# Kernel tuning notes

Hardware: AMD Instinct MI355X
Metric: run time of the kernel (lower is better)

Reference implementation:

```python
import jax, jax.numpy as jnp
import numpy as np

N = 8192
IN_F = 256
HEADS = 4
HF = 64            # head_features = out_features / heads
OUT_F = HEADS * HF # concat=True
NEG_SLOPE = 0.2


def setup_inputs() -> dict:
    key = jax.random.key(0)
    ks = jax.random.split(key, 7)
    x = jax.random.normal(ks[0], (N, IN_F), dtype=jnp.float32)
    graph = jax.random.randint(ks[1], (N, N), 0, 2, dtype=jnp.int32)
    weight = jax.random.normal(ks[2], (HEADS, IN_F, HF), dtype=jnp.float32) * (1.0 / np.sqrt(IN_F))
    weight_i = jax.random.normal(ks[3], (HEADS, HF, 1), dtype=jnp.float32) * (1.0 / np.sqrt(HF))
    weight_j = jax.random.normal(ks[4], (HEADS, HF, 1), dtype=jnp.float32) * (1.0 / np.sqrt(HF))
    weight_r = jax.random.normal(ks[5], (IN_F, HF * HEADS), dtype=jnp.float32) * (1.0 / np.sqrt(IN_F))
    bias = jnp.zeros((OUT_F,), dtype=jnp.float32)
    return {"x": x, "graph": graph, "weight": weight, "weight_i": weight_i,
            "weight_j": weight_j, "weight_r": weight_r, "bias": bias}


def reference(x, graph, weight, weight_i, weight_j, weight_r, bias):
    # h: per-head projected features [heads, N, hf]
    h = jnp.einsum('nm,hmf->hnf', x, weight)
    # additive attention logits: coe_i [h,N,1] + coe_j [h,1,N]
    coe_i = jnp.einsum('hnf,hfo->hno', h, weight_i)          # [heads, N, 1]
    coe_j = jnp.einsum('hnf,hfo->hno', h, weight_j)          # [heads, N, 1]
    coe = jax.nn.leaky_relu(coe_i + jnp.swapaxes(coe_j, 1, 2), NEG_SLOPE)  # [heads, N, N]
    # adjacency mask (note transpose, matching the torch code)
    mask = jnp.where(graph > 0, 0.0, -jnp.inf).T             # [N, N]
    att = jax.nn.softmax(coe + mask[None], axis=-1)          # [heads, N, N]
    # aggregate and move heads to axis 1: [N, heads, hf]
    y = jnp.einsum('hij,hjf->ihf', att, h)
    # residual with projection (in_features != head_features)
    y = y + (x @ weight_r).reshape(N, HEADS, HF)
    # concat heads + bias
    y = y.reshape(N, OUT_F) + bias
    return y
```

## Files before the change

kernel.cpp:

```cpp
#include <hip/hip_runtime.h>
#include <hip/hip_bf16.h>

#define N 8192
#define IN_F 256
#define HEADS 4
#define HF 64
#define OUT_F 256

typedef __attribute__((ext_vector_type(8))) short short8;
typedef __attribute__((ext_vector_type(4))) float f32x4;

__device__ __forceinline__ float lrelu(float x) {
    return fmaxf(x, 0.0f) * 0.8f + x * 0.2f;
}
__device__ __forceinline__ short f2bf(float f) {
    union { __hip_bfloat16 h; short s; } u;
    u.h = __float2bfloat16(f);
    return u.s;
}
__device__ __forceinline__ float bf2f(unsigned short b) {
    union { unsigned u; float f; } v; v.u = ((unsigned)b) << 16;
    return v.f;
}
__device__ __forceinline__ unsigned pack_bf16(float p0, float p1) {
    union { __hip_bfloat162 b; unsigned u; } cv;
    cv.b = __float22bfloat162_rn(make_float2(p0, p1));
    return cv.u;
}

__global__ __launch_bounds__(256) void k_wcvt(
    const float* __restrict__ w, const float* __restrict__ wr,
    unsigned short* __restrict__ BbT)
{
    int c = blockIdx.x;
    int k = threadIdx.x;
    float v;
    if (c < 256) {
        int head = c >> 6, f = c & 63;
        v = w[((size_t)head * IN_F + k) * HF + f];
    } else {
        v = wr[(size_t)k * OUT_F + (c - 256)];
    }
    BbT[(size_t)c * IN_F + k] = (unsigned short)f2bf(v);
}

__global__ __launch_bounds__(256) void k_gemm(
    const float* __restrict__ x, const unsigned short* __restrict__ BbT,
    const float* __restrict__ bias,
    unsigned short* __restrict__ hT, float* __restrict__ out)
{
    __shared__ unsigned short Asw[64 * 64];
    __shared__ unsigned short Bsw[128 * 64];
    int t = threadIdx.x;
    int m0 = blockIdx.x * 64;
    int bn = blockIdx.y;
    int w_ = t >> 6, l = t & 63;
    int wr_ = w_ >> 1, wc_ = w_ & 1;
    int ar = l & 15, g = l >> 4;

    f32x4 acc[2][4];
    #pragma unroll
    for (int m = 0; m < 2; ++m)
        #pragma unroll
        for (int n = 0; n < 4; ++n) acc[m][n] = (f32x4){0.f, 0.f, 0.f, 0.f};

    int srow = t >> 2, skq = (t & 3) * 16;
    int sc = t >> 1, sh = (t & 1) * 32;

    for (int kt = 0; kt < 4; ++kt) {
        const float* xs = x + (size_t)(m0 + srow) * IN_F + kt * 64 + skq;
        float4 xa = ((const float4*)xs)[0];
        float4 xb = ((const float4*)xs)[1];
        float4 xc = ((const float4*)xs)[2];
        float4 xd = ((const float4*)xs)[3];
        unsigned ae[8];
        ae[0] = pack_bf16(xa.x, xa.y); ae[1] = pack_bf16(xa.z, xa.w);
        ae[2] = pack_bf16(xb.x, xb.y); ae[3] = pack_bf16(xb.z, xb.w);
        ae[4] = pack_bf16(xc.x, xc.y); ae[5] = pack_bf16(xc.z, xc.w);
        ae[6] = pack_bf16(xd.x, xd.y); ae[7] = pack_bf16(xd.z, xd.w);
        int kb0 = (skq >> 3) ^ (srow & 7);
        int kb1 = ((skq >> 3) + 1) ^ (srow & 7);
        *(uint4*)&Asw[srow * 64 + kb0 * 8] = *(uint4*)&ae[0];
        *(uint4*)&Asw[srow * 64 + kb1 * 8] = *(uint4*)&ae[4];
        const unsigned short* bs = BbT + (size_t)(bn * 128 + sc) * IN_F + kt * 64 + sh;
        uint4 b0 = ((const uint4*)bs)[0];
        uint4 b1 = ((const uint4*)bs)[1];
        uint4 b2 = ((const uint4*)bs)[2];
        uint4 b3 = ((const uint4*)bs)[3];
        int hb = sh >> 3;
        *(uint4*)&Bsw[sc * 64 + ((hb + 0) ^ (sc & 7)) * 8] = b0;
        *(uint4*)&Bsw[sc * 64 + ((hb + 1) ^ (sc & 7)) * 8] = b1;
        *(uint4*)&Bsw[sc * 64 + ((hb + 2) ^ (sc & 7)) * 8] = b2;
        *(uint4*)&Bsw[sc * 64 + ((hb + 3) ^ (sc & 7)) * 8] = b3;
        __syncthreads();
        #pragma unroll
        for (int ks = 0; ks < 2; ++ks) {
            short8 af[2], bf[4];
            #pragma unroll
            for (int m = 0; m < 2; ++m) {
                int row = wr_ * 32 + m * 16 + ar;
                int kb = (ks * 4 + g) ^ (row & 7);
                af[m] = *(const short8*)&Asw[row * 64 + kb * 8];
            }
            #pragma unroll
            for (int n = 0; n < 4; ++n) {
                int c = wc_ * 64 + n * 16 + ar;
                int kb = (ks * 4 + g) ^ (c & 7);
                bf[n] = *(const short8*)&Bsw[c * 64 + kb * 8];
            }
            #pragma unroll
            for (int m = 0; m < 2; ++m)
                #pragma unroll
                for (int n = 0; n < 4; ++n)
                    acc[m][n] = __builtin_amdgcn_mfma_f32_16x16x32_bf16(af[m], bf[n], acc[m][n], 0, 0, 0);
        }
        __syncthreads();
    }
    #pragma unroll
    for (int m = 0; m < 2; ++m) {
        #pragma unroll
        for (int n = 0; n < 4; ++n) {
            int cg = bn * 128 + wc_ * 64 + n * 16 + ar;
            int mg0 = m0 + wr_ * 32 + m * 16 + g * 4;
            if (cg < 256) {
                int head = cg >> 6, f = cg & 63;
                unsigned pk[2];
                pk[0] = pack_bf16(acc[m][n][0], acc[m][n][1]);
                pk[1] = pack_bf16(acc[m][n][2], acc[m][n][3]);
                *(uint2*)(hT + (size_t)(head * HF + f) * N + mg0) = *(uint2*)pk;
            } else {
                float bb = bias[cg - 256];
                #pragma unroll
                for (int r = 0; r < 4; ++r)
                    out[(size_t)(mg0 + r) * OUT_F + (cg - 256)] = acc[m][n][r] + bb;
            }
        }
    }
}

__global__ __launch_bounds__(256) void k_coe(
    const unsigned short* __restrict__ hT, const float* __restrict__ wi,
    const float* __restrict__ wj, float* __restrict__ coe_i, float* __restrict__ coe_j)
{
    int head = blockIdx.y;
    int n = blockIdx.x * 256 + threadIdx.x;
    const unsigned short* hp = hT + (size_t)head * HF * N + n;
    float si = 0.f, sj = 0.f;
    #pragma unroll 8
    for (int f = 0; f < HF; ++f) {
        float hv = bf2f(hp[(size_t)f * N]);
        si = fmaf(hv, wi[head * HF + f], si);
        sj = fmaf(hv, wj[head * HF + f], sj);
    }
    coe_i[head * N + n] = si;
    coe_j[head * N + n] = sj;
}

__global__ __launch_bounds__(256) void k_cols(
    const float* __restrict__ coe_j, float* __restrict__ maxB,
    float* __restrict__ F, float* __restrict__ H)
{
    __shared__ float red[256];
    int head = blockIdx.x;
    int t = threadIdx.x;
    float m = -1e30f;
    for (int n = t; n < N; n += 256) {
        float b = coe_j[head * N + n];
        F[head * N + n] = __expf(b);
        H[head * N + n] = __expf(0.2f * b);
        m = fmaxf(m, b);
    }
    red[t] = m;
    __syncthreads();
    for (int s = 128; s > 0; s >>= 1) {
        if (t < s) red[t] = fmaxf(red[t], red[t + s]);
        __syncthreads();
    }
    if (t == 0) maxB[head] = red[0];
}

__global__ __launch_bounds__(256) void k_pack(
    const int* __restrict__ graph, unsigned int* __restrict__ bits)
{
    int i = blockIdx.y * 256 + threadIdx.x;
    int jw = blockIdx.x;
    const int* gp = graph + (size_t)(jw * 32) * N + i;
    unsigned int word = 0;
    #pragma unroll
    for (int k = 0; k < 32; ++k)
        word |= (gp[(size_t)k * N] > 0 ? 1u : 0u) << k;
    bits[(size_t)jw * N + i] = word;
}

__device__ __forceinline__ short8 makeP(
    const float4& fa, const float4& fb4, const float4& ha, const float4& hb4,
    unsigned int mk, float Ei, float Gi)
{
    float fv[8] = {fa.x, fa.y, fa.z, fa.w, fb4.x, fb4.y, fb4.z, fb4.w};
    float hv[8] = {ha.x, ha.y, ha.z, ha.w, hb4.x, hb4.y, hb4.z, hb4.w};
    union { short8 s8; unsigned u[4]; } A;
    #pragma unroll
    for (int jp = 0; jp < 4; ++jp) {
        float p0 = fmaxf(Ei * fv[2 * jp],     Gi * hv[2 * jp]);
        float p1 = fmaxf(Ei * fv[2 * jp + 1], Gi * hv[2 * jp + 1]);
        int s0 = ((int)(mk << (31 - 2 * jp))) >> 31;
        int s1 = ((int)(mk << (30 - 2 * jp))) >> 31;
        p0 = __int_as_float(__float_as_int(p0) & s0);
        p1 = __int_as_float(__float_as_int(p1) & s1);
        A.u[jp] = pack_bf16(p0, p1);
    }
    return A.s8;
}

__global__ __launch_bounds__(512) void k_att(
    const unsigned short* __restrict__ hT, const float* __restrict__ coe_i,
    const float* __restrict__ maxB, const float* __restrict__ F,
    const float* __restrict__ H, const unsigned int* __restrict__ bits,
    float* __restrict__ out)
{
    __shared__ char smem[65536];
    unsigned short* hb = (unsigned short*)smem;
    float* mbuf = (float*)smem;

    int t = threadIdx.x;
    int head = blockIdx.y;
    int i0 = blockIdx.x * 64;
    int w = t >> 6, l = t & 63;
    int rg = w >> 2, grp = w & 3;
    int ar = l & 15, g = l >> 4, g8 = g * 8;

    int irow0 = i0 + rg * 32 + ar;
    int irow1 = irow0 + 16;
    float mB = maxB[head];
    float a0 = coe_i[head * N + irow0];
    float a1 = coe_i[head * N + irow1];
    float M0 = lrelu(a0 + mB);
    float M1 = lrelu(a1 + mB);
    float Ei0 = __expf(a0 - M0), Gi0 = __expf(0.2f * a0 - M0);
    float Ei1 = __expf(a1 - M1), Gi1 = __expf(0.2f * a1 - M1);

    f32x4 acc0[4], acc1[4];
    #pragma unroll
    for (int fb = 0; fb < 4; ++fb) {
        acc0[fb] = (f32x4){0.f, 0.f, 0.f, 0.f};
        acc1[fb] = (f32x4){0.f, 0.f, 0.f, 0.f};
    }
    f32x4 accd0 = (f32x4){0.f, 0.f, 0.f, 0.f};
    f32x4 accd1 = (f32x4){0.f, 0.f, 0.f, 0.f};

    short8 ones;
    #pragma unroll
    for (int k = 0; k < 8; ++k) ones[k] = (short)0x3F80;

    int grp_s = t >> 7;
    int v = t & 127;
    int sf = v >> 1;
    int gsel = v & 1;
    const unsigned short* hsrc = hT + ((size_t)(head * HF + sf) * N) + grp_s * 64 + gsel * 32;
    int sfk = sf & 7;
    int wbase = grp_s * 4096 + sf * 64;
    int pgA = ((gsel * 4 + 0) ^ sfk) * 8;
    int pgB = ((gsel * 4 + 1) ^ sfk) * 8;
    int pgC = ((gsel * 4 + 2) ^ sfk) * 8;
    int pgD = ((gsel * 4 + 3) ^ sfk) * 8;

    const float* Fp = F + head * N + g8;
    const float* Hp = H + head * N + g8;
    const unsigned int* bp0 = bits + irow0;
    const unsigned int* bp1 = bits + irow1;

    uint4 hv0 = *(const uint4*)(hsrc + 0);
    uint4 hv1 = *(const uint4*)(hsrc + 8);
    uint4 hv2 = *(const uint4*)(hsrc + 16);
    uint4 hv3 = *(const uint4*)(hsrc + 24);

    for (int s = 0; s < 32; ++s) {
        int jt = s * 256 + grp * 64;
        size_t jw = (size_t)(jt >> 5);
        unsigned int mk00 = bp0[jw * N] >> g8;
        unsigned int mk01 = bp0[(jw + 1) * N] >> g8;
        unsigned int mk10 = bp1[jw * N] >> g8;
        unsigned int mk11 = bp1[(jw + 1) * N] >> g8;
        int bo = (s & 1) * 16384;
        *(uint4*)&hb[bo + wbase + pgA] = hv0;
        *(uint4*)&hb[bo + wbase + pgB] = hv1;
        *(uint4*)&hb[bo + wbase + pgC] = hv2;
        *(uint4*)&hb[bo + wbase + pgD] = hv3;
        int sn = (s + 1 < 32) ? s + 1 : s;
        const unsigned short* hn = hsrc + (size_t)sn * 256;
        hv0 = *(const uint4*)(hn + 0);
        hv1 = *(const uint4*)(hn + 8);
        hv2 = *(const uint4*)(hn + 16);
        hv3 = *(const uint4*)(hn + 24);

        float4 fa0 = *(const float4*)(Fp + jt);
        float4 fb0 = *(const float4*)(Fp + jt + 4);
        float4 ha0 = *(const float4*)(Hp + jt);
        float4 hb0 = *(const float4*)(Hp + jt + 4);
        short8 af00 = makeP(fa0, fb0, ha0, hb0, mk00, Ei0, Gi0);
        short8 af10 = makeP(fa0, fb0, ha0, hb0, mk10, Ei1, Gi1);
        float4 fa1 = *(const float4*)(Fp + jt + 32);
        float4 fb1 = *(const float4*)(Fp + jt + 36);
        float4 ha1 = *(const float4*)(Hp + jt + 32);
        float4 hb1 = *(const float4*)(Hp + jt + 36);
        short8 af01 = makeP(fa1, fb1, ha1, hb1, mk01, Ei0, Gi0);
        short8 af11 = makeP(fa1, fb1, ha1, hb1, mk11, Ei1, Gi1);

        __syncthreads();

        const unsigned short* rb = &hb[bo + grp * 4096];
        #pragma unroll
        for (int ss = 0; ss < 2; ++ss) {
            short8 a0f = ss ? af01 : af00;
            short8 a1f = ss ? af11 : af10;
            #pragma unroll
            for (int fb = 0; fb < 4; ++fb) {
                int row = fb * 16 + ar;
                int pg = (ss * 4 + g) ^ (ar & 7);
                short8 bfr = *(const short8*)&rb[row * 64 + pg * 8];
                acc0[fb] = __builtin_amdgcn_mfma_f32_16x16x32_bf16(a0f, bfr, acc0[fb], 0, 0, 0);
                acc1[fb] = __builtin_amdgcn_mfma_f32_16x16x32_bf16(a1f, bfr, acc1[fb], 0, 0, 0);
            }
            accd0 = __builtin_amdgcn_mfma_f32_16x16x32_bf16(a0f, ones, accd0, 0, 0, 0);
            accd1 = __builtin_amdgcn_mfma_f32_16x16x32_bf16(a1f, ones, accd1, 0, 0, 0);
        }
    }

    __syncthreads();
    int slot = rg * 64 + l;
    if (grp > 0) {
        float* dst = mbuf + (size_t)(grp - 1) * 5248 + slot * 41;
        #pragma unroll
        for (int fb = 0; fb < 4; ++fb)
            #pragma unroll
            for (int r = 0; r < 4; ++r) {
                dst[fb * 4 + r] = acc0[fb][r];
                dst[16 + fb * 4 + r] = acc1[fb][r];
            }
        #pragma unroll
        for (int r = 0; r < 4; ++r) {
            dst[32 + r] = accd0[r];
            dst[36 + r] = accd1[r];
        }
    }
    __syncthreads();
    if (grp == 0) {
        #pragma unroll
        for (int q = 0; q < 3; ++q) {
            const float* src = mbuf + (size_t)q * 5248 + slot * 41;
            #pragma unroll
            for (int fb = 0; fb < 4; ++fb)
                #pragma unroll
                for (int r = 0; r < 4; ++r) {
                    acc0[fb][r] += src[fb * 4 + r];
                    acc1[fb][r] += src[16 + fb * 4 + r];
                }
            #pragma unroll
            for (int r = 0; r < 4; ++r) {
                accd0[r] += src[32 + r];
                accd1[r] += src[36 + r];
            }
        }
        #pragma unroll
        for (int r = 0; r < 4; ++r) {
            float inv0 = 1.0f / accd0[r];
            float inv1 = 1.0f / accd1[r];
            int orow0 = i0 + rg * 32 + g * 4 + r;
            float* op0 = out + (size_t)orow0 * OUT_F + head * HF + ar;
            float* op1 = op0 + 16 * OUT_F;
            #pragma unroll
            for (int fb = 0; fb < 4; ++fb) {
                op0[fb * 16] += acc0[fb][r] * inv0;
                op1[fb * 16] += acc1[fb][r] * inv1;
            }
        }
    }
}

extern "C" void kernel_launch(void* const* d_in, const int* in_sizes, int n_in,
                              void* d_out, int out_size, void* d_ws, size_t ws_size,
                              hipStream_t stream) {
    const float* x     = (const float*)d_in[0];
    const int*   graph = (const int*)d_in[1];
    const float* w     = (const float*)d_in[2];
    const float* wi    = (const float*)d_in[3];
    const float* wj    = (const float*)d_in[4];
    const float* wr    = (const float*)d_in[5];
    const float* bias  = (const float*)d_in[6];
    float* out = (float*)d_out;

    char* ws = (char*)d_ws;
    unsigned short* hT  = (unsigned short*)(ws);
    float* coe_i = (float*)(ws + 4194304);
    float* coe_j = (float*)(ws + 4325376);
    float* maxB  = (float*)(ws + 4456448);
    float* F     = (float*)(ws + 4457472);
    float* H     = (float*)(ws + 4588544);
    unsigned short* BbT = (unsigned short*)(ws + 4719616);
    unsigned int* bits  = (unsigned int*)(ws + 4981760);

    k_wcvt<<<dim3(512), 256, 0, stream>>>(w, wr, BbT);
    k_gemm<<<dim3(128, 4), 256, 0, stream>>>(x, BbT, bias, hT, out);
    k_coe<<<dim3(32, 4), 256, 0, stream>>>(hT, wi, wj, coe_i, coe_j);
    k_cols<<<dim3(4), 256, 0, stream>>>(coe_j, maxB, F, H);
    k_pack<<<dim3(256, 32), 256, 0, stream>>>(graph, bits);
    k_att<<<dim3(N / 64, HEADS), 512, 0, stream>>>(hT, coe_i, maxB, F, H, bits, out);
}
```

Measured before the change: 169.1 us.

## Split attention key dimension across two blocks and normalize in a separate kernel

The attention kernel now splits the N key columns into two halves via blockIdx.z. Each block uses 256 threads (4 waves) instead of 512 and half the LDS, and writes unnormalized numerators and denominators to workspace. A new k_norm kernel sums the two partials, divides, and adds the result to the output. This raises block count and lowers the in-block cross-wave reduction, with the aim of better occupancy and load balance. The cost is an extra kernel launch and a round trip of partial sums through global memory.

Result: slower. 211.0 us (+24.8%).

```diff
diff --git a/kernel.cpp b/kernel.cpp
--- a/kernel.cpp
+++ b/kernel.cpp
@@ -212,21 +212,23 @@
     return A.s8;
 }
 
-__global__ __launch_bounds__(512) void k_att(
+__global__ __launch_bounds__(256) void k_att(
     const unsigned short* __restrict__ hT, const float* __restrict__ coe_i,
     const float* __restrict__ maxB, const float* __restrict__ F,
     const float* __restrict__ H, const unsigned int* __restrict__ bits,
-    float* __restrict__ out)
-{
-    __shared__ char smem[65536];
+    float* __restrict__ num, float* __restrict__ den)
+{
+    __shared__ char smem[32768];
     unsigned short* hb = (unsigned short*)smem;
     float* mbuf = (float*)smem;
 
     int t = threadIdx.x;
     int head = blockIdx.y;
     int i0 = blockIdx.x * 64;
+    int kc = blockIdx.z;
+    int jbase = kc * (N / 2);
     int w = t >> 6, l = t & 63;
-    int rg = w >> 2, grp = w & 3;
+    int rg = w >> 1, grp = w & 1;
     int ar = l & 15, g = l >> 4, g8 = g * 8;
 
     int irow0 = i0 + rg * 32 + ar;
@@ -256,7 +258,7 @@
     int v = t & 127;
     int sf = v >> 1;
     int gsel = v & 1;
-    const unsigned short* hsrc = hT + ((size_t)(head * HF + sf) * N) + grp_s * 64 + gsel * 32;
+    const unsigned short* hsrc = hT + ((size_t)(head * HF + sf) * N) + jbase + grp_s * 64 + gsel * 32;
     int sfk = sf & 7;
     int wbase = grp_s * 4096 + sf * 64;
     int pgA = ((gsel * 4 + 0) ^ sfk) * 8;
@@ -275,19 +277,19 @@
     uint4 hv3 = *(const uint4*)(hsrc + 24);
 
     for (int s = 0; s < 32; ++s) {
-        int jt = s * 256 + grp * 64;
-        size_t jw = (size_t)(jt >> 5);
-        unsigned int mk00 = bp0[jw * N] >> g8;
-        unsigned int mk01 = bp0[(jw + 1) * N] >> g8;
-        unsigned int mk10 = bp1[jw * N] >> g8;
-        unsigned int mk11 = bp1[(jw + 1) * N] >> g8;
-        int bo = (s & 1) * 16384;
+        int jt = jbase + s * 128 + grp * 64;
+        size_t jwd = (size_t)(jt >> 5);
+        unsigned int mk00 = bp0[jwd * N] >> g8;
+        unsigned int mk01 = bp0[(jwd + 1) * N] >> g8;
+        unsigned int mk10 = bp1[jwd * N] >> g8;
+        unsigned int mk11 = bp1[(jwd + 1) * N] >> g8;
+        int bo = (s & 1) * 8192;
         *(uint4*)&hb[bo + wbase + pgA] = hv0;
         *(uint4*)&hb[bo + wbase + pgB] = hv1;
         *(uint4*)&hb[bo + wbase + pgC] = hv2;
         *(uint4*)&hb[bo + wbase + pgD] = hv3;
         int sn = (s + 1 < 32) ? s + 1 : s;
-        const unsigned short* hn = hsrc + (size_t)sn * 256;
+        const unsigned short* hn = hsrc + (size_t)sn * 128;
         hv0 = *(const uint4*)(hn + 0);
         hv1 = *(const uint4*)(hn + 8);
         hv2 = *(const uint4*)(hn + 16);
@@ -328,8 +330,8 @@
 
     __syncthreads();
     int slot = rg * 64 + l;
-    if (grp > 0) {
-        float* dst = mbuf + (size_t)(grp - 1) * 5248 + slot * 41;
+    if (grp == 1) {
+        float* dst = mbuf + (size_t)slot * 41;
         #pragma unroll
         for (int fb = 0; fb < 4; ++fb)
             #pragma unroll
@@ -345,36 +347,50 @@
     }
     __syncthreads();
     if (grp == 0) {
-        #pragma unroll
-        for (int q = 0; q < 3; ++q) {
-            const float* src = mbuf + (size_t)q * 5248 + slot * 41;
-            #pragma unroll
-            for (int fb = 0; fb < 4; ++fb)
-                #pragma unroll
-                for (int r = 0; r < 4; ++r) {
-                    acc0[fb][r] += src[fb * 4 + r];
-                    acc1[fb][r] += src[16 + fb * 4 + r];
-                }
+        const float* src = mbuf + (size_t)slot * 41;
+        #pragma unroll
+        for (int fb = 0; fb < 4; ++fb)
             #pragma unroll
             for (int r = 0; r < 4; ++r) {
-                accd0[r] += src[32 + r];
-                accd1[r] += src[36 + r];
-            }
-        }
+                acc0[fb][r] += src[fb * 4 + r];
+                acc1[fb][r] += src[16 + fb * 4 + r];
+            }
         #pragma unroll
         for (int r = 0; r < 4; ++r) {
-            float inv0 = 1.0f / accd0[r];
-            float inv1 = 1.0f / accd1[r];
+            accd0[r] += src[32 + r];
+            accd1[r] += src[36 + r];
+        }
+        size_t base = (size_t)(kc * HEADS + head) * N;
+        #pragma unroll
+        for (int r = 0; r < 4; ++r) {
             int orow0 = i0 + rg * 32 + g * 4 + r;
-            float* op0 = out + (size_t)orow0 * OUT_F + head * HF + ar;
-            float* op1 = op0 + 16 * OUT_F;
+            float* np0 = num + (base + orow0) * HF + ar;
+            float* np1 = np0 + 16 * HF;
             #pragma unroll
             for (int fb = 0; fb < 4; ++fb) {
-                op0[fb * 16] += acc0[fb][r] * inv0;
-                op1[fb * 16] += acc1[fb][r] * inv1;
-            }
-        }
-    }
+                np0[fb * 16] = acc0[fb][r];
+                np1[fb * 16] = acc1[fb][r];
+            }
+            if (ar == 0) {
+                den[base + orow0] = accd0[r];
+                den[base + orow0 + 16] = accd1[r];
+            }
+        }
+    }
+}
+
+__global__ __launch_bounds__(256) void k_norm(
+    const float* __restrict__ num, const float* __restrict__ den,
+    float* __restrict__ out)
+{
+    int n = blockIdx.x;
+    int c = threadIdx.x;
+    int head = c >> 6, f = c & 63;
+    size_t b0 = (size_t)head * N + n;
+    size_t b1 = (size_t)(HEADS + head) * N + n;
+    float v = num[b0 * HF + f] + num[b1 * HF + f];
+    float d = den[b0] + den[b1];
+    out[(size_t)n * OUT_F + c] += v / d;
 }
 
 extern "C" void kernel_launch(void* const* d_in, const int* in_sizes, int n_in,
@@ -398,11 +414,14 @@
     float* H     = (float*)(ws + 4588544);
     unsigned short* BbT = (unsigned short*)(ws + 4719616);
     unsigned int* bits  = (unsigned int*)(ws + 4981760);
+    float* num = (float*)(ws + (size_t)(16u << 20));
+    float* den = (float*)(ws + (size_t)(33u << 20));
 
     k_wcvt<<<dim3(512), 256, 0, stream>>>(w, wr, BbT);
     k_gemm<<<dim3(128, 4), 256, 0, stream>>>(x, BbT, bias, hT, out);
     k_coe<<<dim3(32, 4), 256, 0, stream>>>(hT, wi, wj, coe_i, coe_j);
     k_cols<<<dim3(4), 256, 0, stream>>>(coe_j, maxB, F, H);
     k_pack<<<dim3(256, 32), 256, 0, stream>>>(graph, bits);
-    k_att<<<dim3(N / 64, HEADS), 512, 0, stream>>>(hT, coe_i, maxB, F, H, bits, out);
-}
+    k_att<<<dim3(N / 64, HEADS, 2), 256, 0, stream>>>(hT, coe_i, maxB, F, H, bits, num, den);
+    k_norm<<<dim3(N), 256, 0, stream>>>(num, den, out);
+}
```

## Read hT B-fragments directly from global, split j range per wave, remap blocks

Applied to the files above, without the earlier changes.

Removes the LDS double-buffered staging of the transposed h tile and its per-iteration __syncthreads. Each wave now loads its MFMA B fragments straight from global memory and walks its own contiguous quarter of the j range. Block indices are remapped so neighbouring blocks share a head and adjacent row tiles, which should improve L2 reuse of hT, F and H. The cost is more global/L2 traffic, with uncoalesced-ish 16-byte loads strided by N and no cooperative reuse across the waves of a block.

Measured after the change: 238.3 us. 1.41x slower.

```diff
diff --git a/kernel.cpp b/kernel.cpp
--- a/kernel.cpp
+++ b/kernel.cpp
@@ -218,15 +218,16 @@
     const float* __restrict__ H, const unsigned int* __restrict__ bits,
     float* __restrict__ out)
 {
-    __shared__ char smem[65536];
-    unsigned short* hb = (unsigned short*)smem;
-    float* mbuf = (float*)smem;
+    __shared__ float mbuf[3 * 128 * 41];
 
     int t = threadIdx.x;
-    int head = blockIdx.y;
-    int i0 = blockIdx.x * 64;
+    int bid = blockIdx.x + gridDim.x * blockIdx.y;
+    int head = (bid >> 1) & 3;
+    int i_idx = ((bid >> 3) << 1) | (bid & 1);
+    int i0 = i_idx * 64;
+
     int w = t >> 6, l = t & 63;
-    int rg = w >> 2, grp = w & 3;
+    int rg = w >> 2, jq = w & 3;
     int ar = l & 15, g = l >> 4, g8 = g * 8;
 
     int irow0 = i0 + rg * 32 + ar;
@@ -252,72 +253,43 @@
     #pragma unroll
     for (int k = 0; k < 8; ++k) ones[k] = (short)0x3F80;
 
-    int grp_s = t >> 7;
-    int v = t & 127;
-    int sf = v >> 1;
-    int gsel = v & 1;
-    const unsigned short* hsrc = hT + ((size_t)(head * HF + sf) * N) + grp_s * 64 + gsel * 32;
-    int sfk = sf & 7;
-    int wbase = grp_s * 4096 + sf * 64;
-    int pgA = ((gsel * 4 + 0) ^ sfk) * 8;
-    int pgB = ((gsel * 4 + 1) ^ sfk) * 8;
-    int pgC = ((gsel * 4 + 2) ^ sfk) * 8;
-    int pgD = ((gsel * 4 + 3) ^ sfk) * 8;
-
     const float* Fp = F + head * N + g8;
     const float* Hp = H + head * N + g8;
     const unsigned int* bp0 = bits + irow0;
     const unsigned int* bp1 = bits + irow1;
-
-    uint4 hv0 = *(const uint4*)(hsrc + 0);
-    uint4 hv1 = *(const uint4*)(hsrc + 8);
-    uint4 hv2 = *(const uint4*)(hsrc + 16);
-    uint4 hv3 = *(const uint4*)(hsrc + 24);
-
-    for (int s = 0; s < 32; ++s) {
-        int jt = s * 256 + grp * 64;
-        size_t jw = (size_t)(jt >> 5);
-        unsigned int mk00 = bp0[jw * N] >> g8;
-        unsigned int mk01 = bp0[(jw + 1) * N] >> g8;
-        unsigned int mk10 = bp1[jw * N] >> g8;
-        unsigned int mk11 = bp1[(jw + 1) * N] >> g8;
-        int bo = (s & 1) * 16384;
-        *(uint4*)&hb[bo + wbase + pgA] = hv0;
-        *(uint4*)&hb[bo + wbase + pgB] = hv1;
-        *(uint4*)&hb[bo + wbase + pgC] = hv2;
-        *(uint4*)&hb[bo + wbase + pgD] = hv3;
-        int sn = (s + 1 < 32) ? s + 1 : s;
-        const unsigned short* hn = hsrc + (size_t)sn * 256;
-        hv0 = *(const uint4*)(hn + 0);
-        hv1 = *(const uint4*)(hn + 8);
-        hv2 = *(const uint4*)(hn + 16);
-        hv3 = *(const uint4*)(hn + 24);
-
+    const unsigned short* hB = hT + ((size_t)(head * HF + ar) * N) + g8;
+
+    int j0 = jq * (N / 4);
+    int j1 = j0 + (N / 4);
+
+    for (int jt = j0; jt < j1; jt += 64) {
+        size_t jwd = (size_t)(jt >> 5);
+        unsigned int mk00 = bp0[jwd * N] >> g8;
+        unsigned int mk01 = bp0[(jwd + 1) * N] >> g8;
+        unsigned int mk10 = bp1[jwd * N] >> g8;
+        unsigned int mk11 = bp1[(jwd + 1) * N] >> g8;
         float4 fa0 = *(const float4*)(Fp + jt);
         float4 fb0 = *(const float4*)(Fp + jt + 4);
         float4 ha0 = *(const float4*)(Hp + jt);
         float4 hb0 = *(const float4*)(Hp + jt + 4);
-        short8 af00 = makeP(fa0, fb0, ha0, hb0, mk00, Ei0, Gi0);
-        short8 af10 = makeP(fa0, fb0, ha0, hb0, mk10, Ei1, Gi1);
         float4 fa1 = *(const float4*)(Fp + jt + 32);
         float4 fb1 = *(const float4*)(Fp + jt + 36);
         float4 ha1 = *(const float4*)(Hp + jt + 32);
         float4 hb1 = *(const float4*)(Hp + jt + 36);
+
+        short8 af00 = makeP(fa0, fb0, ha0, hb0, mk00, Ei0, Gi0);
+        short8 af10 = makeP(fa0, fb0, ha0, hb0, mk10, Ei1, Gi1);
         short8 af01 = makeP(fa1, fb1, ha1, hb1, mk01, Ei0, Gi0);
         short8 af11 = makeP(fa1, fb1, ha1, hb1, mk11, Ei1, Gi1);
 
-        __syncthreads();
-
-        const unsigned short* rb = &hb[bo + grp * 4096];
         #pragma unroll
         for (int ss = 0; ss < 2; ++ss) {
             short8 a0f = ss ? af01 : af00;
             short8 a1f = ss ? af11 : af10;
+            const unsigned short* hs = hB + jt + ss * 32;
             #pragma unroll
             for (int fb = 0; fb < 4; ++fb) {
-                int row = fb * 16 + ar;
-                int pg = (ss * 4 + g) ^ (ar & 7);
-                short8 bfr = *(const short8*)&rb[row * 64 + pg * 8];
+                short8 bfr = *(const short8*)(hs + (size_t)(fb * 16) * N);
                 acc0[fb] = __builtin_amdgcn_mfma_f32_16x16x32_bf16(a0f, bfr, acc0[fb], 0, 0, 0);
                 acc1[fb] = __builtin_amdgcn_mfma_f32_16x16x32_bf16(a1f, bfr, acc1[fb], 0, 0, 0);
             }
@@ -326,10 +298,9 @@
         }
     }
 
-    __syncthreads();
     int slot = rg * 64 + l;
-    if (grp > 0) {
-        float* dst = mbuf + (size_t)(grp - 1) * 5248 + slot * 41;
+    if (jq > 0) {
+        float* dst = mbuf + (size_t)(jq - 1) * 5248 + slot * 41;
         #pragma unroll
         for (int fb = 0; fb < 4; ++fb)
             #pragma unroll
@@ -344,7 +315,7 @@
         }
     }
     __syncthreads();
-    if (grp == 0) {
+    if (jq == 0) {
         #pragma unroll
         for (int q = 0; q < 3; ++q) {
             const float* src = mbuf + (size_t)q * 5248 + slot * 41;
```

## Merge graph bit-packing into GEMM launch and prefetch mask words in attention loop

Applied to the files above, without the earlier changes.

Folds the graph bit-packing kernel into the GEMM kernel as extra blocks, so the memory-bound 256MB graph read can overlap with the projection GEMM in a single launch. In the attention kernel, mask words for the next step are prefetched a full iteration ahead and F/H loads are moved earlier. The __syncthreads is replaced by an explicit lgkmcnt wait, s_barrier and sched_barrier, and mask bit extraction now uses sbfe. This adds register pressure from the prefetched mask words, and the hand-rolled barrier changes how the compiler schedules around it.

Result: slower. 174.7 us (+3.3%).

```diff
diff --git a/kernel.cpp b/kernel.cpp
--- a/kernel.cpp
+++ b/kernel.cpp
@@ -44,16 +44,32 @@
     BbT[(size_t)c * IN_F + k] = (unsigned short)f2bf(v);
 }
 
-__global__ __launch_bounds__(256) void k_gemm(
+__global__ __launch_bounds__(256) void k_gemm_pack(
     const float* __restrict__ x, const unsigned short* __restrict__ BbT,
     const float* __restrict__ bias,
-    unsigned short* __restrict__ hT, float* __restrict__ out)
+    unsigned short* __restrict__ hT, float* __restrict__ out,
+    const int* __restrict__ graph, unsigned int* __restrict__ bits)
 {
     __shared__ unsigned short Asw[64 * 64];
     __shared__ unsigned short Bsw[128 * 64];
+    int b = blockIdx.x;
     int t = threadIdx.x;
-    int m0 = blockIdx.x * 64;
-    int bn = blockIdx.y;
+
+    if (b >= 512) {
+        int p = b - 512;
+        int jw = p & 255;
+        int i = (p >> 8) * 256 + t;
+        const int* gp = graph + (size_t)(jw * 32) * N + i;
+        unsigned int word = 0;
+        #pragma unroll
+        for (int k = 0; k < 32; ++k)
+            word |= (gp[(size_t)k * N] > 0 ? 1u : 0u) << k;
+        bits[(size_t)jw * N + i] = word;
+        return;
+    }
+
+    int m0 = (b & 127) * 64;
+    int bn = b >> 7;
     int w_ = t >> 6, l = t & 63;
     int wr_ = w_ >> 1, wc_ = w_ & 1;
     int ar = l & 15, g = l >> 4;
@@ -179,19 +195,6 @@
     if (t == 0) maxB[head] = red[0];
 }
 
-__global__ __launch_bounds__(256) void k_pack(
-    const int* __restrict__ graph, unsigned int* __restrict__ bits)
-{
-    int i = blockIdx.y * 256 + threadIdx.x;
-    int jw = blockIdx.x;
-    const int* gp = graph + (size_t)(jw * 32) * N + i;
-    unsigned int word = 0;
-    #pragma unroll
-    for (int k = 0; k < 32; ++k)
-        word |= (gp[(size_t)k * N] > 0 ? 1u : 0u) << k;
-    bits[(size_t)jw * N + i] = word;
-}
-
 __device__ __forceinline__ short8 makeP(
     const float4& fa, const float4& fb4, const float4& ha, const float4& hb4,
     unsigned int mk, float Ei, float Gi)
@@ -203,8 +206,8 @@
     for (int jp = 0; jp < 4; ++jp) {
         float p0 = fmaxf(Ei * fv[2 * jp],     Gi * hv[2 * jp]);
         float p1 = fmaxf(Ei * fv[2 * jp + 1], Gi * hv[2 * jp + 1]);
-        int s0 = ((int)(mk << (31 - 2 * jp))) >> 31;
-        int s1 = ((int)(mk << (30 - 2 * jp))) >> 31;
+        int s0 = __builtin_amdgcn_sbfe((int)mk, 2 * jp, 1);
+        int s1 = __builtin_amdgcn_sbfe((int)mk, 2 * jp + 1, 1);
         p0 = __int_as_float(__float_as_int(p0) & s0);
         p1 = __int_as_float(__float_as_int(p1) & s1);
         A.u[jp] = pack_bf16(p0, p1);
@@ -273,14 +276,23 @@
     uint4 hv1 = *(const uint4*)(hsrc + 8);
     uint4 hv2 = *(const uint4*)(hsrc + 16);
     uint4 hv3 = *(const uint4*)(hsrc + 24);
+    int jt0 = grp * 64;
+    size_t jw0 = (size_t)(jt0 >> 5);
+    unsigned int mk00 = bp0[jw0 * N] >> g8;
+    unsigned int mk01 = bp0[(jw0 + 1) * N] >> g8;
+    unsigned int mk10 = bp1[jw0 * N] >> g8;
+    unsigned int mk11 = bp1[(jw0 + 1) * N] >> g8;
 
     for (int s = 0; s < 32; ++s) {
         int jt = s * 256 + grp * 64;
-        size_t jw = (size_t)(jt >> 5);
-        unsigned int mk00 = bp0[jw * N] >> g8;
-        unsigned int mk01 = bp0[(jw + 1) * N] >> g8;
-        unsigned int mk10 = bp1[jw * N] >> g8;
-        unsigned int mk11 = bp1[(jw + 1) * N] >> g8;
+        float4 fa0 = *(const float4*)(Fp + jt);
+        float4 fb0 = *(const float4*)(Fp + jt + 4);
+        float4 ha0 = *(const float4*)(Hp + jt);
+        float4 hb0 = *(const float4*)(Hp + jt + 4);
+        float4 fa1 = *(const float4*)(Fp + jt + 32);
+        float4 fb1 = *(const float4*)(Fp + jt + 36);
+        float4 ha1 = *(const float4*)(Hp + jt + 32);
+        float4 hb1 = *(const float4*)(Hp + jt + 36);
         int bo = (s & 1) * 16384;
         *(uint4*)&hb[bo + wbase + pgA] = hv0;
         *(uint4*)&hb[bo + wbase + pgB] = hv1;
@@ -292,22 +304,19 @@
         hv1 = *(const uint4*)(hn + 8);
         hv2 = *(const uint4*)(hn + 16);
         hv3 = *(const uint4*)(hn + 24);
-
-        float4 fa0 = *(const float4*)(Fp + jt);
-        float4 fb0 = *(const float4*)(Fp + jt + 4);
-        float4 ha0 = *(const float4*)(Hp + jt);
-        float4 hb0 = *(const float4*)(Hp + jt + 4);
+        int jtn = sn * 256 + grp * 64;
+        size_t jwn = (size_t)(jtn >> 5);
+        unsigned int nk00 = bp0[jwn * N] >> g8;
+        unsigned int nk01 = bp0[(jwn + 1) * N] >> g8;
+        unsigned int nk10 = bp1[jwn * N] >> g8;
+        unsigned int nk11 = bp1[(jwn + 1) * N] >> g8;
         short8 af00 = makeP(fa0, fb0, ha0, hb0, mk00, Ei0, Gi0);
         short8 af10 = makeP(fa0, fb0, ha0, hb0, mk10, Ei1, Gi1);
-        float4 fa1 = *(const float4*)(Fp + jt + 32);
-        float4 fb1 = *(const float4*)(Fp + jt + 36);
-        float4 ha1 = *(const float4*)(Hp + jt + 32);
-        float4 hb1 = *(const float4*)(Hp + jt + 36);
         short8 af01 = makeP(fa1, fb1, ha1, hb1, mk01, Ei0, Gi0);
         short8 af11 = makeP(fa1, fb1, ha1, hb1, mk11, Ei1, Gi1);
-
-        __syncthreads();
-
+        asm volatile("s_waitcnt lgkmcnt(0)" ::: "memory");
+        __builtin_amdgcn_s_barrier();
+        __builtin_amdgcn_sched_barrier(0);
         const unsigned short* rb = &hb[bo + grp * 4096];
         #pragma unroll
         for (int ss = 0; ss < 2; ++ss) {
@@ -324,6 +333,7 @@
             accd0 = __builtin_amdgcn_mfma_f32_16x16x32_bf16(a0f, ones, accd0, 0, 0, 0);
             accd1 = __builtin_amdgcn_mfma_f32_16x16x32_bf16(a1f, ones, accd1, 0, 0, 0);
         }
+        mk00 = nk00; mk01 = nk01; mk10 = nk10; mk11 = nk11;
     }
 
     __syncthreads();
@@ -400,9 +410,8 @@
     unsigned int* bits  = (unsigned int*)(ws + 4981760);
 
     k_wcvt<<<dim3(512), 256, 0, stream>>>(w, wr, BbT);
-    k_gemm<<<dim3(128, 4), 256, 0, stream>>>(x, BbT, bias, hT, out);
+    k_gemm_pack<<<dim3(512 + 8192), 256, 0, stream>>>(x, BbT, bias, hT, out, graph, bits);
     k_coe<<<dim3(32, 4), 256, 0, stream>>>(hT, wi, wj, coe_i, coe_j);
     k_cols<<<dim3(4), 256, 0, stream>>>(coe_j, maxB, F, H);
-    k_pack<<<dim3(256, 32), 256, 0, stream>>>(graph, bits);
     k_att<<<dim3(N / 64, HEADS), 512, 0, stream>>>(hT, coe_i, maxB, F, H, bits, out);
 }
```
